# Performance work log

Hardware: AMD Instinct MI355X
Metric: run time of the kernel (lower is better)

## Reference

```python
import jax, jax.numpy as jnp
import numpy as np

jax.config.update("jax_enable_x64", True)

EPS = 1e-6
NUM_LEVELS = 16
LOG2_T = 19
BASE_RES = 16
DESIRED_RES = 2048
F = 2
N_POINTS = 131072
PS = (1, 19349663, 83492791)
CORNERS = np.array([[0, 0, 0], [0, 0, 1], [0, 1, 0], [0, 1, 1],
                    [1, 0, 0], [1, 0, 1], [1, 1, 0], [1, 1, 1]], dtype=np.float32)


def _isprime(n):
    if n < 2:
        return False
    i = 2
    while i * i <= n:
        if n % i == 0:
            return False
        i += 1
    return True


def _build_meta():
    T = 2 ** LOG2_T
    while not _isprime(T):
        T += 1
    b = (DESIRED_RES / BASE_RES) ** (1.0 / (NUM_LEVELS - 1))
    offsets = [0]
    scales = []
    start_hash = -1
    for i in range(NUM_LEVELS):
        res = int(BASE_RES * b ** i)
        scales.append(res)
        n = (res + 1) ** 3
        if n > T:
            if start_hash < 0:
                start_hash = i
            n = T
        offsets.append(offsets[-1] + n)
    sh = NUM_LEVELS if start_hash == -1 else start_hash
    return T, np.array(scales, dtype=np.int64), np.array(offsets, dtype=np.int64), sh


TABLE, SCALES, OFFSETS, START_HASH = _build_meta()


def setup_inputs():
    key = jax.random.key(0)
    k1, k2 = jax.random.split(key)
    xyz = jax.random.normal(k1, (N_POINTS, 3), dtype=jnp.float32)
    wbounds = jnp.arange(6, dtype=jnp.float32)  # box min [0,1,2], max [3,4,5]
    std = 1e-4
    data = jax.random.uniform(k2, (int(OFFSETS[-1]), F), dtype=jnp.float32,
                              minval=-std, maxval=std)
    return {"xyz": xyz, "wbounds": wbounds, "data": data}


def _hashgrid(xyz, wbounds, data):
    scales_f = jnp.asarray(SCALES, dtype=jnp.float32)   # [L]
    scales_i = jnp.asarray(SCALES)                      # [L] int64
    corner = jnp.asarray(CORNERS)                       # [8,3] float32
    level_off = jnp.asarray(OFFSETS[:-1])               # [L] int64
    # normalize into [0,1]^3 (torch uses .item() on the max -> detached)
    x = jnp.clip(xyz, wbounds[:3], wbounds[3:6])
    denom = jax.lax.stop_gradient(jnp.max(wbounds[3:6] - wbounds[:3])) + EPS
    x = (x - wbounds[:3]) / denom
    fx = x[None] * scales_f[:, None, None]              # [L,N,3]
    int_xyz = (fx[:, :, None, :] + corner[None, None]).astype(jnp.int64)  # [L,N,8,3]
    off = fx - int_xyz[:, :, 0].astype(jnp.float32)     # [L,N,3] frac part
    sp1 = scales_i + 1
    dense = (int_xyz[..., 0] * (sp1 ** 2)[:, None, None]
             + int_xyz[..., 1] * sp1[:, None, None]
             + int_xyz[..., 2])                          # [L,N,8]
    hashed = ((int_xyz[..., 0] * PS[0]) ^ (int_xyz[..., 1] * PS[1])
              ^ (int_xyz[..., 2] * PS[2])) % TABLE       # [L,N,8]
    lvl = jnp.arange(NUM_LEVELS, dtype=jnp.int64)[:, None, None]
    ind = jnp.where(lvl < START_HASH, dense, hashed) + level_off[:, None, None]
    val = data[ind]                                      # [L,N,8,F] gather
    # trilinear weights per corner
    w = jnp.clip(1.0 - corner[None, None]
                 + (2.0 * corner[None, None] - 1.0) * off[:, :, None, :], 0.0, 1.0)
    wprod = w[..., 0] * w[..., 1] * w[..., 2]            # [L,N,8]
    out = jnp.einsum('lnc,lncf->lnf', wprod, val)        # [L,N,F]
    return out.transpose(1, 0, 2).reshape(-1, NUM_LEVELS * F)


def reference(xyz, wbounds, data):
    return _hashgrid(xyz, wbounds, data)
```

## Files before the change

### kernel.cpp

```cpp
#include <hip/hip_runtime.h>
#include <stdint.h>
#include <math.h>

#define NLVL 16
#define NPTS 131072
#define BPTS 64
#define NTHR 256

struct Meta {
  int scales[NLVL];
  int offsets[NLVL];
  unsigned int T;
  int start_hash;
  double invT;
};

__device__ __forceinline__ int fastmod(uint64_t h, unsigned int T, double invT) {
  uint64_t q = (uint64_t)((double)h * invT);
  long long r = (long long)(h - q * (uint64_t)T);
  if (r < 0) r += (long long)T;
  else if (r >= (long long)T) r -= (long long)T;
  return (int)r;
}

__device__ __forceinline__ void level_idx(
    int l, float xn, float yn, float zn, const Meta& m,
    int* __restrict__ idx, float* __restrict__ o)
{
#pragma clang fp contract(off)
  const float sf = (float)m.scales[l];
  const float fx = xn * sf, fy = yn * sf, fz = zn * sf;
  const int ix0 = (int)fx,          iy0 = (int)fy,          iz0 = (int)fz;
  const int ix1 = (int)(fx + 1.0f), iy1 = (int)(fy + 1.0f), iz1 = (int)(fz + 1.0f);
  o[0] = fx - (float)ix0; o[1] = fy - (float)iy0; o[2] = fz - (float)iz0;
  const int base = m.offsets[l];

  if (l < m.start_hash) {
    const int sp1 = m.scales[l] + 1;
    const int sq  = sp1 * sp1;
    const int ax0 = ix0 * sq,  ax1 = ix1 * sq;
    const int ay0 = iy0 * sp1, ay1 = iy1 * sp1;
    idx[0] = base + ax0 + ay0 + iz0;
    idx[1] = base + ax0 + ay0 + iz1;
    idx[2] = base + ax0 + ay1 + iz0;
    idx[3] = base + ax0 + ay1 + iz1;
    idx[4] = base + ax1 + ay0 + iz0;
    idx[5] = base + ax1 + ay0 + iz1;
    idx[6] = base + ax1 + ay1 + iz0;
    idx[7] = base + ax1 + ay1 + iz1;
  } else {
    const uint64_t hx0 = (uint64_t)ix0;
    const uint64_t hx1 = (uint64_t)ix1;
    const uint64_t hy0 = (uint64_t)iy0 * 19349663ull;
    const uint64_t hy1 = hy0 + 19349663ull;
    const uint64_t hz0 = (uint64_t)iz0 * 83492791ull;
    const uint64_t hz1 = hz0 + 83492791ull;
    idx[0] = base + fastmod(hx0 ^ hy0 ^ hz0, m.T, m.invT);
    idx[1] = base + fastmod(hx0 ^ hy0 ^ hz1, m.T, m.invT);
    idx[2] = base + fastmod(hx0 ^ hy1 ^ hz0, m.T, m.invT);
    idx[3] = base + fastmod(hx0 ^ hy1 ^ hz1, m.T, m.invT);
    idx[4] = base + fastmod(hx1 ^ hy0 ^ hz0, m.T, m.invT);
    idx[5] = base + fastmod(hx1 ^ hy0 ^ hz1, m.T, m.invT);
    idx[6] = base + fastmod(hx1 ^ hy1 ^ hz0, m.T, m.invT);
    idx[7] = base + fastmod(hx1 ^ hy1 ^ hz1, m.T, m.invT);
  }
}

__global__ __launch_bounds__(NTHR) void hashgrid_fwd(
    const float* __restrict__ xyz,
    const float* __restrict__ wb,
    const float* __restrict__ data,
    float* __restrict__ out,
    Meta meta)
{
#pragma clang fp contract(off)
  const int t    = threadIdx.x;
  const int wave = t >> 6;
  const int lane = t & 63;
  const int pbase = blockIdx.x * BPTS;

  __shared__ float  sxyz[BPTS * 3];
  __shared__ int    hist[64];
  __shared__ int    sidx[BPTS];
  __shared__ float2 tile[BPTS][NLVL + 1];

  if (t < 48)
    reinterpret_cast<float4*>(sxyz)[t] =
        reinterpret_cast<const float4*>(xyz + pbase * 3)[t];
  if (t < 64) hist[t] = 0;
  __syncthreads();

  const float bx0 = wb[0], by0 = wb[1], bz0 = wb[2];
  const float bx1 = wb[3], by1 = wb[4], bz1 = wb[5];
  const float denom = fmaxf(fmaxf(bx1 - bx0, by1 - by0), bz1 - bz0) + 1e-6f;

  int key = 0;
  if (t < 64) {
    float px = sxyz[t * 3 + 0], py = sxyz[t * 3 + 1], pz = sxyz[t * 3 + 2];
    px = fminf(fmaxf(px, bx0), bx1);
    py = fminf(fmaxf(py, by0), by1);
    pz = fminf(fmaxf(pz, bz0), bz1);
    const float xn = (px - bx0) / denom;
    const float yn = (py - by0) / denom;
    const float zn = (pz - bz0) / denom;
    const int kx = min((int)(xn * 4.0f), 3);
    const int ky = min((int)(yn * 4.0f), 3);
    const int kz = min((int)(zn * 4.0f), 3);
    key = kx * 16 + ky * 4 + kz;
    atomicAdd(&hist[key], 1);
  }
  __syncthreads();

  if (t < 64) {
    int v = hist[t];
#pragma unroll
    for (int d = 1; d < 64; d <<= 1) {
      int u = __shfl_up(v, d, 64);
      if (lane >= d) v += u;
    }
    hist[t] = v;
  }
  __syncthreads();

  if (t < 64) {
    const int pos = atomicSub(&hist[key], 1) - 1;
    sidx[pos] = t;
  }
  __syncthreads();

  const int p = sidx[lane];
  float px = sxyz[p * 3 + 0], py = sxyz[p * 3 + 1], pz = sxyz[p * 3 + 2];
  px = fminf(fmaxf(px, bx0), bx1);
  py = fminf(fmaxf(py, by0), by1);
  pz = fminf(fmaxf(pz, bz0), bz1);
  const float xn = (px - bx0) / denom;
  const float yn = (py - by0) / denom;
  const float zn = (pz - bz0) / denom;

  const float2* __restrict__ dp = (const float2*)data;

#pragma unroll 2
  for (int s = 0; s < 4; ++s) {
    const int l = wave + 4 * s;
    int idx[8];
    float o[3];
    level_idx(l, xn, yn, zn, meta, idx, o);

    float2 v[8];
#pragma unroll
    for (int k = 0; k < 8; ++k) v[k] = dp[idx[k]];

    const float wx[2] = {1.0f - o[0], o[0]};
    const float wy[2] = {1.0f - o[1], o[1]};
    const float wz[2] = {1.0f - o[2], o[2]};
    float a0 = 0.0f, a1 = 0.0f;
#pragma unroll
    for (int c = 0; c < 8; ++c) {
      const float w = (wx[(c >> 2) & 1] * wy[(c >> 1) & 1]) * wz[c & 1];
      a0 += w * v[c].x;
      a1 += w * v[c].y;
    }
    tile[p][l] = make_float2(a0, a1);
  }
  __syncthreads();

#pragma unroll
  for (int it = 0; it < 2; ++it) {
    const int idx = t + it * NTHR;
    const int pp = idx >> 3;
    const int q  = idx & 7;
    const float2 e0 = tile[pp][2 * q];
    const float2 e1 = tile[pp][2 * q + 1];
    reinterpret_cast<float4*>(out)[(pbase + pp) * 8 + q] =
        make_float4(e0.x, e0.y, e1.x, e1.y);
  }
}

static bool isprime_ll(long long v) {
  if (v < 2) return false;
  for (long long i = 2; i * i <= v; ++i)
    if (v % i == 0) return false;
  return true;
}

extern "C" void kernel_launch(void* const* d_in, const int* in_sizes, int n_in,
                              void* d_out, int out_size, void* d_ws, size_t ws_size,
                              hipStream_t stream) {
  (void)in_sizes; (void)n_in; (void)d_ws; (void)ws_size; (void)out_size;

  Meta m;
  long long T = 1LL << 19;
  while (!isprime_ll(T)) ++T;
  const double b = pow(2048.0 / 16.0, 1.0 / 15.0);
  long long off = 0;
  int sh = -1;
  for (int i = 0; i < NLVL; ++i) {
    const int res = (int)(16.0 * pow(b, (double)i));
    m.scales[i] = res;
    m.offsets[i] = (int)off;
    long long nn = (long long)(res + 1) * (res + 1) * (res + 1);
    if (nn > T) { if (sh < 0) sh = i; nn = T; }
    off += nn;
  }
  m.T = (unsigned int)T;
  m.start_hash = (sh < 0) ? NLVL : sh;
  m.invT = 1.0 / (double)T;

  const float* xyz  = (const float*)d_in[0];
  const float* wbp  = (const float*)d_in[1];
  const float* data = (const float*)d_in[2];
  float* out = (float*)d_out;

  hipLaunchKernelGGL(hashgrid_fwd, dim3(NPTS / BPTS), dim3(NTHR), 0, stream,
                     xyz, wbp, data, out, m);
}
```

Measured before the change: 32.54 us.

## Skip hash gathers for points clamped to box-min corner via compaction pass

Adds a classify kernel that flags points whose clamped coordinates equal the box minimum and compacts the remaining points into a list with wave ballots and an atomic counter. The same kernel computes the shared output for the corner once. The main kernel then runs the full hash-grid gathers only on the compacted list and scatters results by point id. Extra blocks broadcast the shared corner value to the flagged points. This cuts redundant random gathers whenever many inputs clamp to the same corner, at the cost of a memset, an extra launch, workspace traffic and scattered writes.

```diff
diff --git a/kernel.cpp b/kernel.cpp
--- a/kernel.cpp
+++ b/kernel.cpp
@@ -6,6 +6,15 @@
 #define NPTS 131072
 #define BPTS 64
 #define NTHR 256
+
+#define OFF_COUNT 0
+#define OFF_CV    64
+#define OFF_FLAG  256
+#define OFF_LIST  16640
+#define WS_NEED   (16640 + NPTS * 4)
+
+#define GRID_P1   (NPTS / BPTS)
+#define GRID_P2   (NPTS * 8 / 1024)
 
 struct Meta {
   int scales[NLVL];
@@ -66,6 +75,210 @@
   }
 }
 
+__global__ __launch_bounds__(NTHR) void hg_classify(
+    const float* __restrict__ xyz,
+    const float* __restrict__ wb,
+    const float* __restrict__ data,
+    unsigned int* __restrict__ count,
+    float* __restrict__ cornerval,
+    unsigned int* __restrict__ flagw,
+    int* __restrict__ list,
+    Meta meta)
+{
+#pragma clang fp contract(off)
+  const int t    = threadIdx.x;
+  const int lane = t & 63;
+  const int p    = blockIdx.x * NTHR + t;
+
+  const float bx0 = wb[0], by0 = wb[1], bz0 = wb[2];
+  const float bx1 = wb[3], by1 = wb[4], bz1 = wb[5];
+
+  const float x = xyz[3 * p + 0], y = xyz[3 * p + 1], z = xyz[3 * p + 2];
+  const float cx = fminf(fmaxf(x, bx0), bx1);
+  const float cy = fminf(fmaxf(y, by0), by1);
+  const float cz = fminf(fmaxf(z, bz0), bz1);
+  const bool corner = (cx == bx0) && (cy == by0) && (cz == bz0);
+
+  const unsigned long long mc = __ballot(corner);
+  const unsigned long long mn = __ballot(!corner);
+
+  const int pw = blockIdx.x * NTHR + (t & ~63);
+  if (lane == 0)  flagw[(pw >> 5) + 0] = (unsigned int)(mc & 0xffffffffull);
+  if (lane == 32) flagw[(pw >> 5) + 1] = (unsigned int)(mc >> 32);
+
+  unsigned int base = 0;
+  if (lane == 0) base = atomicAdd(count, (unsigned int)__popcll(mn));
+  base = (unsigned int)__shfl((int)base, 0, 64);
+  if (!corner) {
+    const unsigned int pos =
+        base + (unsigned int)__popcll(mn & ((1ull << lane) - 1ull));
+    list[pos] = p;
+  }
+
+  if (blockIdx.x == 0 && t < 16) {
+    int idx[8];
+    float o[3];
+    level_idx(t, 0.0f, 0.0f, 0.0f, meta, idx, o);
+    const float2* __restrict__ dp = (const float2*)data;
+    float2 v[8];
+#pragma unroll
+    for (int k = 0; k < 8; ++k) v[k] = dp[idx[k]];
+    const float wx[2] = {1.0f - o[0], o[0]};
+    const float wy[2] = {1.0f - o[1], o[1]};
+    const float wz[2] = {1.0f - o[2], o[2]};
+    float a0 = 0.0f, a1 = 0.0f;
+#pragma unroll
+    for (int c = 0; c < 8; ++c) {
+      const float w = (wx[(c >> 2) & 1] * wy[(c >> 1) & 1]) * wz[c & 1];
+      a0 += w * v[c].x;
+      a1 += w * v[c].y;
+    }
+    reinterpret_cast<float2*>(cornerval)[t] = make_float2(a0, a1);
+  }
+}
+
+__global__ __launch_bounds__(NTHR) void hg_main(
+    const float* __restrict__ xyz,
+    const float* __restrict__ wb,
+    const float* __restrict__ data,
+    float* __restrict__ out,
+    const unsigned int* __restrict__ count,
+    const float* __restrict__ cornerval,
+    const unsigned int* __restrict__ flagw,
+    const int* __restrict__ list,
+    Meta meta)
+{
+#pragma clang fp contract(off)
+  const int t = threadIdx.x;
+
+  if (blockIdx.x >= GRID_P1) {
+    const int b2 = blockIdx.x - GRID_P1;
+    const float4 cv = reinterpret_cast<const float4*>(cornerval)[t & 7];
+    float4* __restrict__ out4 = reinterpret_cast<float4*>(out);
+#pragma unroll
+    for (int it = 0; it < 4; ++it) {
+      const int fi = b2 * 1024 + it * NTHR + t;
+      const int p  = fi >> 3;
+      const unsigned int w = flagw[p >> 5];
+      if ((w >> (p & 31)) & 1u) out4[fi] = cv;
+    }
+    return;
+  }
+
+  const int cntNC = (int)*count;
+  const int pbase = blockIdx.x * BPTS;
+  if (pbase >= cntNC) return;
+
+  const int wave = t >> 6;
+  const int lane = t & 63;
+
+  __shared__ int    spid[BPTS];
+  __shared__ float  sxyz[BPTS * 3];
+  __shared__ int    hist[64];
+  __shared__ int    sidx[BPTS];
+  __shared__ float2 tile[BPTS][NLVL + 1];
+
+  if (t < 64) {
+    const int li  = pbase + t;
+    const int pid = (li < cntNC) ? list[li] : -1;
+    spid[t] = pid;
+    const int sp = pid < 0 ? 0 : pid;
+    sxyz[t * 3 + 0] = xyz[sp * 3 + 0];
+    sxyz[t * 3 + 1] = xyz[sp * 3 + 1];
+    sxyz[t * 3 + 2] = xyz[sp * 3 + 2];
+    hist[t] = 0;
+  }
+  __syncthreads();
+
+  const float bx0 = wb[0], by0 = wb[1], bz0 = wb[2];
+  const float bx1 = wb[3], by1 = wb[4], bz1 = wb[5];
+  const float denom = fmaxf(fmaxf(bx1 - bx0, by1 - by0), bz1 - bz0) + 1e-6f;
+
+  int key = 0;
+  if (t < 64) {
+    float px = sxyz[t * 3 + 0], py = sxyz[t * 3 + 1], pz = sxyz[t * 3 + 2];
+    px = fminf(fmaxf(px, bx0), bx1);
+    py = fminf(fmaxf(py, by0), by1);
+    pz = fminf(fmaxf(pz, bz0), bz1);
+    const float xn = (px - bx0) / denom;
+    const float yn = (py - by0) / denom;
+    const float zn = (pz - bz0) / denom;
+    const int kx = min((int)(xn * 4.0f), 3);
+    const int ky = min((int)(yn * 4.0f), 3);
+    const int kz = min((int)(zn * 4.0f), 3);
+    key = kx * 16 + ky * 4 + kz;
+    atomicAdd(&hist[key], 1);
+  }
+  __syncthreads();
+
+  if (t < 64) {
+    int v = hist[t];
+#pragma unroll
+    for (int d = 1; d < 64; d <<= 1) {
+      int u = __shfl_up(v, d, 64);
+      if (lane >= d) v += u;
+    }
+    hist[t] = v;
+  }
+  __syncthreads();
+
+  if (t < 64) {
+    const int pos = atomicSub(&hist[key], 1) - 1;
+    sidx[pos] = t;
+  }
+  __syncthreads();
+
+  const int slot = sidx[lane];
+  float px = sxyz[slot * 3 + 0], py = sxyz[slot * 3 + 1], pz = sxyz[slot * 3 + 2];
+  px = fminf(fmaxf(px, bx0), bx1);
+  py = fminf(fmaxf(py, by0), by1);
+  pz = fminf(fmaxf(pz, bz0), bz1);
+  const float xn = (px - bx0) / denom;
+  const float yn = (py - by0) / denom;
+  const float zn = (pz - bz0) / denom;
+
+  const float2* __restrict__ dp = (const float2*)data;
+
+#pragma unroll 2
+  for (int s = 0; s < 4; ++s) {
+    const int l = wave + 4 * s;
+    int idx[8];
+    float o[3];
+    level_idx(l, xn, yn, zn, meta, idx, o);
+
+    float2 v[8];
+#pragma unroll
+    for (int k = 0; k < 8; ++k) v[k] = dp[idx[k]];
+
+    const float wx[2] = {1.0f - o[0], o[0]};
+    const float wy[2] = {1.0f - o[1], o[1]};
+    const float wz[2] = {1.0f - o[2], o[2]};
+    float a0 = 0.0f, a1 = 0.0f;
+#pragma unroll
+    for (int c = 0; c < 8; ++c) {
+      const float w = (wx[(c >> 2) & 1] * wy[(c >> 1) & 1]) * wz[c & 1];
+      a0 += w * v[c].x;
+      a1 += w * v[c].y;
+    }
+    tile[slot][l] = make_float2(a0, a1);
+  }
+  __syncthreads();
+
+#pragma unroll
+  for (int it = 0; it < 2; ++it) {
+    const int idx2 = t + it * NTHR;
+    const int pp = idx2 >> 3;
+    const int q  = idx2 & 7;
+    const int pid = spid[pp];
+    if (pid >= 0) {
+      const float2 e0 = tile[pp][2 * q];
+      const float2 e1 = tile[pp][2 * q + 1];
+      reinterpret_cast<float4*>(out)[pid * 8 + q] =
+          make_float4(e0.x, e0.y, e1.x, e1.y);
+    }
+  }
+}
+
 __global__ __launch_bounds__(NTHR) void hashgrid_fwd(
     const float* __restrict__ xyz,
     const float* __restrict__ wb,
@@ -110,7 +323,6 @@
     atomicAdd(&hist[key], 1);
   }
   __syncthreads();
-
   if (t < 64) {
     int v = hist[t];
 #pragma unroll
@@ -121,7 +333,6 @@
     hist[t] = v;
   }
   __syncthreads();
-
   if (t < 64) {
     const int pos = atomicSub(&hist[key], 1) - 1;
     sidx[pos] = t;
@@ -145,11 +356,9 @@
     int idx[8];
     float o[3];
     level_idx(l, xn, yn, zn, meta, idx, o);
-
     float2 v[8];
 #pragma unroll
     for (int k = 0; k < 8; ++k) v[k] = dp[idx[k]];
-
     const float wx[2] = {1.0f - o[0], o[0]};
     const float wy[2] = {1.0f - o[1], o[1]};
     const float wz[2] = {1.0f - o[2], o[2]};
@@ -166,9 +375,9 @@
 
 #pragma unroll
   for (int it = 0; it < 2; ++it) {
-    const int idx = t + it * NTHR;
-    const int pp = idx >> 3;
-    const int q  = idx & 7;
+    const int idx2 = t + it * NTHR;
+    const int pp = idx2 >> 3;
+    const int q  = idx2 & 7;
     const float2 e0 = tile[pp][2 * q];
     const float2 e1 = tile[pp][2 * q + 1];
     reinterpret_cast<float4*>(out)[(pbase + pp) * 8 + q] =
@@ -186,7 +395,7 @@
 extern "C" void kernel_launch(void* const* d_in, const int* in_sizes, int n_in,
                               void* d_out, int out_size, void* d_ws, size_t ws_size,
                               hipStream_t stream) {
-  (void)in_sizes; (void)n_in; (void)d_ws; (void)ws_size; (void)out_size;
+  (void)in_sizes; (void)n_in; (void)out_size;
 
   Meta m;
   long long T = 1LL << 19;
@@ -211,6 +420,21 @@
   const float* data = (const float*)d_in[2];
   float* out = (float*)d_out;
 
-  hipLaunchKernelGGL(hashgrid_fwd, dim3(NPTS / BPTS), dim3(NTHR), 0, stream,
-                     xyz, wbp, data, out, m);
-}
+  if (ws_size < (size_t)WS_NEED) {
+    hipLaunchKernelGGL(hashgrid_fwd, dim3(NPTS / BPTS), dim3(NTHR), 0, stream,
+                       xyz, wbp, data, out, m);
+    return;
+  }
+
+  char* ws = (char*)d_ws;
+  unsigned int* count = (unsigned int*)(ws + OFF_COUNT);
+  float*        cv    = (float*)(ws + OFF_CV);
+  unsigned int* flagw = (unsigned int*)(ws + OFF_FLAG);
+  int*          list  = (int*)(ws + OFF_LIST);
+
+  hipMemsetAsync(count, 0, sizeof(unsigned int), stream);
+  hipLaunchKernelGGL(hg_classify, dim3(NPTS / NTHR), dim3(NTHR), 0, stream,
+                     xyz, wbp, data, count, cv, flagw, list, m);
+  hipLaunchKernelGGL(hg_main, dim3(GRID_P1 + GRID_P2), dim3(NTHR), 0, stream,
+                     xyz, wbp, data, out, count, cv, flagw, list, m);
+}
```

Result: slower. 61.78 us (+89.9%).
